# Kernel tuning notes

Hardware: AMD Instinct MI355X
Metric: run time of the kernel (lower is better)

Reference implementation:

```python
import jax, jax.numpy as jnp
import numpy as np

TOPK, NUM_CLASSES, ALPHA, BETA = 13, 80, 1.0, 6.0
IOU_EPS = 1e-7


def _cxcywh_to_xyxy(b):
    cx, cy, w, h = b[..., 0], b[..., 1], b[..., 2], b[..., 3]
    return cx - w / 2, cy - h / 2, cx + w / 2, cy + h / 2


def _pairwise_iou(pd, gt):
    # pd: [B,A,4] cxcywh, gt: [B,G,4] cxcywh -> iou [B,A,G]
    p1x, p1y, p2x, p2y = _cxcywh_to_xyxy(pd)
    g1x, g1y, g2x, g2y = _cxcywh_to_xyxy(gt)
    ix1 = jnp.maximum(p1x[:, :, None], g1x[:, None, :])
    iy1 = jnp.maximum(p1y[:, :, None], g1y[:, None, :])
    ix2 = jnp.minimum(p2x[:, :, None], g2x[:, None, :])
    iy2 = jnp.minimum(p2y[:, :, None], g2y[:, None, :])
    inter = jnp.clip(ix2 - ix1, 0) * jnp.clip(iy2 - iy1, 0)
    area_p = (p2x - p1x) * (p2y - p1y)  # [B,A]
    area_g = (g2x - g1x) * (g2y - g1y)  # [B,G]
    union = area_p[:, :, None] + area_g[:, None, :] - inter + IOU_EPS
    return inter / union


def setup_inputs() -> dict:
    key = jax.random.key(0)
    ks = jax.random.split(key, 8)
    B, A, G, C = 32, 8400, 64, 80
    img = 640.0
    pd_scores = jax.random.normal(ks[0], (B, A, C), dtype=jnp.float32)
    pd_cxy = jax.random.uniform(ks[1], (B, A, 2)) * img
    pd_wh = jax.random.uniform(ks[2], (B, A, 2)) * 115.0 + 5.0
    pd_bboxes = jnp.concatenate([pd_cxy, pd_wh], axis=-1).astype(jnp.float32)
    anc_points = (jax.random.uniform(ks[3], (A, 2)) * img).astype(jnp.float32)
    gt_labels = jax.random.randint(ks[4], (B, G, 1), 0, C, dtype=jnp.int32)
    gt_cxy = jax.random.uniform(ks[5], (B, G, 2)) * img
    gt_wh = jax.random.uniform(ks[6], (B, G, 2)) * 115.0 + 5.0
    gt_bboxes = jnp.concatenate([gt_cxy, gt_wh], axis=-1).astype(jnp.float32)
    mask_gt = jax.random.uniform(ks[7], (B, G, 1)) < 0.7  # bool
    return {"pd_scores": pd_scores, "pd_bboxes": pd_bboxes, "anc_points": anc_points,
            "gt_labels": gt_labels, "gt_bboxes": gt_bboxes, "mask_gt": mask_gt}


def reference(pd_scores, pd_bboxes, anc_points, gt_labels, gt_bboxes, mask_gt):
    B, A, C = pd_scores.shape
    G = gt_bboxes.shape[1]
    valid = mask_gt[..., 0].astype(bool)          # [B,G]
    labels = gt_labels[..., 0].astype(jnp.int32)  # [B,G]

    overlaps = _pairwise_iou(pd_bboxes, gt_bboxes)                 # [B,A,G]
    onehot_gt = jax.nn.one_hot(labels, C, dtype=pd_scores.dtype)   # [B,G,C]
    score_gt = jnp.einsum('bac,bgc->bag', pd_scores, onehot_gt)    # gather score at gt class
    metrics = jax.nn.sigmoid(score_gt) ** ALPHA * overlaps ** BETA  # [B,A,G], >= 0
    metrics = jnp.where(valid[:, None, :], metrics, -1.0)          # invalid gt -> sentinel

    # top-k anchors per gt (dim over anchors)
    _, topk_idx = jax.lax.top_k(jnp.swapaxes(metrics, 1, 2), TOPK)  # [B,G,k]
    b_ix = jnp.arange(B)[:, None, None]
    g_ix = jnp.arange(G)[None, :, None]
    cand = jnp.zeros((B, A, G), dtype=bool).at[b_ix, topk_idx, g_ix].set(True)
    cand = cand & valid[:, None, :]

    # (last such gt under ties, matching sequential overwrite order);
    # otherwise the first candidate gt keeps the anchor.
    anchor_max = metrics.max(axis=-1)                               # [B,A]
    is_max_cand = (metrics >= anchor_max[..., None]) & cand         # [B,A,G]
    has_max = is_max_cand.any(axis=-1)
    last_max = (G - 1) - jnp.argmax(is_max_cand[:, :, ::-1].astype(jnp.int32), axis=-1)
    first_cand = jnp.argmax(cand.astype(jnp.int32), axis=-1)
    assigned = jnp.where(has_max, last_max, first_cand)             # [B,A]
    fg = cand.any(axis=-1)                                          # [B,A] bool

    asg_label = jnp.take_along_axis(labels, assigned, axis=1)                   # [B,A]
    asg_bbox = jnp.take_along_axis(gt_bboxes, assigned[:, :, None], axis=1)     # [B,A,4]
    asg_iou = jnp.take_along_axis(overlaps, assigned[:, :, None], axis=2)[..., 0]  # [B,A]

    oh = jax.nn.one_hot(asg_label, C, dtype=pd_scores.dtype)
    fgf = fg.astype(pd_scores.dtype)
    target_labels = oh * fgf[..., None]
    target_bboxes = asg_bbox * fgf[..., None]
    target_scores = oh * (asg_iou * fgf)[..., None]
    return target_labels, target_bboxes, target_scores, fg
```

## Files before the change

kernel.cpp:

```cpp
#include <hip/hip_runtime.h>

#define NB 32
#define NA 8400
#define NG 64
#define NC 80
#define NK 13
#define TILE0 64
#define NT0 132

#define OFF_LBL  0
#define OFF_BBOX 21504000
#define OFF_SCR  22579200
#define OFF_FG   44083200

#define WS_METRICS_OFF 0
#define WS_METRICS_SZ  (32ull*64*8400*4)
#define WS_MASK_OFF    WS_METRICS_SZ
#define WS_MASK_SZ     (32ull*8400*8)
#define WS_NEEDED      (WS_METRICS_SZ + WS_MASK_SZ)

__device__ __forceinline__ float sigmoid_f(float x) {
    return 1.0f / (1.0f + expf(-x));
}

__device__ __forceinline__ float iou_corners(
    float px1, float py1, float px2, float py2, float ap,
    float gx1, float gy1, float gx2, float gy2, float ag)
{
    float ix1 = fmaxf(px1, gx1), iy1 = fmaxf(py1, gy1);
    float ix2 = fminf(px2, gx2), iy2 = fminf(py2, gy2);
    float inter = fmaxf(ix2 - ix1, 0.0f) * fmaxf(iy2 - iy1, 0.0f);
    return inter / (ap + ag - inter + 1e-7f);
}

__global__ __launch_bounds__(256) void metrics_kernel(
    const float* __restrict__ pd_scores,
    const float* __restrict__ pd_bboxes,
    const int* __restrict__ gt_labels,
    const float* __restrict__ gt_bboxes,
    const int* __restrict__ mask_gt,
    float* __restrict__ metrics)
{
    const int b  = blockIdx.y;
    const int a0 = blockIdx.x * TILE0;
    const int tid = threadIdx.x;
    const int an = min(TILE0, NA - a0);

    __shared__ float s_sc[TILE0 * 81];
    __shared__ float s_pb[TILE0 * 5];
    __shared__ float s_gb[NG * 5];
    __shared__ int   s_lab[NG];
    __shared__ int   s_val[NG];

    const float* sbase = pd_scores + ((size_t)b * NA + a0) * NC;
    for (int i4 = tid; i4 < an * 20; i4 += 256) {
        const float4 v = reinterpret_cast<const float4*>(sbase)[i4];
        const int al = i4 / 20;
        const int c  = (i4 % 20) * 4;
        float* d = &s_sc[al * 81 + c];
        d[0] = sigmoid_f(v.x); d[1] = sigmoid_f(v.y);
        d[2] = sigmoid_f(v.z); d[3] = sigmoid_f(v.w);
    }
    if (tid < an) {
        const float4 pb = *reinterpret_cast<const float4*>(pd_bboxes + ((size_t)b * NA + a0 + tid) * 4);
        const float px1 = pb.x - pb.z * 0.5f, py1 = pb.y - pb.w * 0.5f;
        const float px2 = pb.x + pb.z * 0.5f, py2 = pb.y + pb.w * 0.5f;
        s_pb[tid * 5 + 0] = px1; s_pb[tid * 5 + 1] = py1;
        s_pb[tid * 5 + 2] = px2; s_pb[tid * 5 + 3] = py2;
        s_pb[tid * 5 + 4] = (px2 - px1) * (py2 - py1);
    }
    if (tid >= 64 && tid < 64 + NG) {
        const int g = tid - 64;
        const float4 gb = *reinterpret_cast<const float4*>(gt_bboxes + ((size_t)b * NG + g) * 4);
        const float gx1 = gb.x - gb.z * 0.5f, gy1 = gb.y - gb.w * 0.5f;
        const float gx2 = gb.x + gb.z * 0.5f, gy2 = gb.y + gb.w * 0.5f;
        s_gb[g * 5 + 0] = gx1; s_gb[g * 5 + 1] = gy1;
        s_gb[g * 5 + 2] = gx2; s_gb[g * 5 + 3] = gy2;
        s_gb[g * 5 + 4] = (gx2 - gx1) * (gy2 - gy1);
        s_lab[g] = gt_labels[b * NG + g];
        s_val[g] = mask_gt[b * NG + g];
    }
    __syncthreads();

    const int a_local = tid & 63;
    const int ggrp    = tid >> 6;
    if (a_local < an) {
        const float px1 = s_pb[a_local * 5 + 0], py1 = s_pb[a_local * 5 + 1];
        const float px2 = s_pb[a_local * 5 + 2], py2 = s_pb[a_local * 5 + 3];
        const float ap  = s_pb[a_local * 5 + 4];
        #pragma unroll 4
        for (int gg = 0; gg < 16; ++gg) {
            const int g = gg * 4 + ggrp;
            float m = -1.0f;
            if (s_val[g]) {
                const float iou = iou_corners(px1, py1, px2, py2, ap,
                                              s_gb[g*5+0], s_gb[g*5+1], s_gb[g*5+2], s_gb[g*5+3], s_gb[g*5+4]);
                const float i2 = iou * iou;
                m = s_sc[a_local * 81 + s_lab[g]] * (i2 * i2 * i2);
            }
            metrics[((size_t)(b * NG + g)) * NA + a0 + a_local] = m;
        }
    }
}

__global__ __launch_bounds__(256) void topk_kernel(
    const float* __restrict__ metrics,
    const int* __restrict__ mask_gt,
    unsigned long long* __restrict__ cand_mask)
{
    const int g = blockIdx.x;
    const int b = blockIdx.y;
    const int tid = threadIdx.x;

    if (mask_gt[b * NG + g] == 0) return;

    __shared__ float sm[NA];
    __shared__ float wv[4];
    __shared__ int   wi[4];
    __shared__ int   s_sel[NK];

    const float* mrow = metrics + (size_t)(b * NG + g) * NA;
    for (int a = tid; a < NA; a += 256) sm[a] = mrow[a];
    __syncthreads();

    for (int k = 0; k < NK; ++k) {
        float bv = -3.0f;
        int   bi = 0x7fffffff;
        for (int a = tid; a < NA; a += 256) {
            const float v = sm[a];
            if (v > bv || (v == bv && a < bi)) { bv = v; bi = a; }
        }
        #pragma unroll
        for (int off = 32; off; off >>= 1) {
            const float ov = __shfl_xor(bv, off);
            const int   oi = __shfl_xor(bi, off);
            if (ov > bv || (ov == bv && oi < bi)) { bv = ov; bi = oi; }
        }
        const int wave = tid >> 6;
        if ((tid & 63) == 0) { wv[wave] = bv; wi[wave] = bi; }
        __syncthreads();
        if (tid == 0) {
            #pragma unroll
            for (int w = 1; w < 4; ++w) {
                if (wv[w] > bv || (wv[w] == bv && wi[w] < bi)) { bv = wv[w]; bi = wi[w]; }
            }
            s_sel[k] = bi;
            sm[bi] = -2.0f;
        }
        __syncthreads();
    }
    if (tid < NK) {
        atomicOr(&cand_mask[(size_t)b * NA + s_sel[tid]], 1ull << g);
    }
}

__global__ __launch_bounds__(256) void assign_kernel(
    const float* __restrict__ metrics,
    const float* __restrict__ pd_bboxes,
    const int* __restrict__ gt_labels,
    const float* __restrict__ gt_bboxes,
    const unsigned long long* __restrict__ cand_mask,
    float* __restrict__ out)
{
    const int b = blockIdx.y;
    const int a0 = blockIdx.x * 256;
    const int tid = threadIdx.x;
    const int a = a0 + tid;
    const bool active = a < NA;

    __shared__ float s_gb[NG * 5];
    __shared__ float s_graw[NG][4];
    __shared__ int   s_lab[NG];
    __shared__ int   s_albl[256];
    __shared__ float s_aiou[256];

    if (tid < NG) {
        const float4 gb = *reinterpret_cast<const float4*>(gt_bboxes + ((size_t)b * NG + tid) * 4);
        s_graw[tid][0] = gb.x; s_graw[tid][1] = gb.y; s_graw[tid][2] = gb.z; s_graw[tid][3] = gb.w;
        const float gx1 = gb.x - gb.z * 0.5f, gy1 = gb.y - gb.w * 0.5f;
        const float gx2 = gb.x + gb.z * 0.5f, gy2 = gb.y + gb.w * 0.5f;
        s_gb[tid * 5 + 0] = gx1; s_gb[tid * 5 + 1] = gy1;
        s_gb[tid * 5 + 2] = gx2; s_gb[tid * 5 + 3] = gy2;
        s_gb[tid * 5 + 4] = (gx2 - gx1) * (gy2 - gy1);
        s_lab[tid] = gt_labels[b * NG + tid];
    }
    __syncthreads();

    unsigned long long cand = 0ull;
    float maxv = -2.0f;
    int   last = -1;
    if (active) {
        cand = cand_mask[(size_t)b * NA + a];
        const float* mcol = metrics + (size_t)b * NG * NA + a;
        for (int g = 0; g < NG; ++g) {
            const float mv = mcol[(size_t)g * NA];
            const bool cb = (cand >> g) & 1ull;
            if (mv > maxv)       { maxv = mv; last = cb ? g : -1; }
            else if (mv == maxv && cb) { last = g; }
        }
    }

    const bool fg = (cand != 0ull);
    int assigned = 0;
    float aiou = 0.0f;
    if (fg) {
        assigned = (last >= 0) ? last : (__ffsll(cand) - 1);
        const float4 pb = *reinterpret_cast<const float4*>(pd_bboxes + ((size_t)b * NA + a) * 4);
        const float px1 = pb.x - pb.z * 0.5f, py1 = pb.y - pb.w * 0.5f;
        const float px2 = pb.x + pb.z * 0.5f, py2 = pb.y + pb.w * 0.5f;
        const float ap = (px2 - px1) * (py2 - py1);
        aiou = iou_corners(px1, py1, px2, py2, ap,
                           s_gb[assigned*5+0], s_gb[assigned*5+1],
                           s_gb[assigned*5+2], s_gb[assigned*5+3], s_gb[assigned*5+4]);
    }

    s_albl[tid] = fg ? s_lab[assigned] : -1;
    s_aiou[tid] = fg ? aiou : 0.0f;

    if (active) {
        float4 ob = fg ? make_float4(s_graw[assigned][0], s_graw[assigned][1],
                                     s_graw[assigned][2], s_graw[assigned][3])
                       : make_float4(0.f, 0.f, 0.f, 0.f);
        *reinterpret_cast<float4*>(out + OFF_BBOX + ((size_t)b * NA + a) * 4) = ob;
        out[OFF_FG + (size_t)b * NA + a] = fg ? 1.0f : 0.0f;
    }
    __syncthreads();

    const int cnt = min(256, NA - a0);
    for (int i = tid; i < cnt * NC; i += 256) {
        const int al = i / NC;
        const int c  = i - al * NC;
        const int lbl = s_albl[al];
        const float lv = (c == lbl) ? 1.0f : 0.0f;
        const float sv = (c == lbl) ? s_aiou[al] : 0.0f;
        const size_t base = ((size_t)b * NA + (a0 + al)) * NC + c;
        out[OFF_LBL + base] = lv;
        out[OFF_SCR + base] = sv;
    }
}

__global__ __launch_bounds__(256) void topk_fb(
    const float* __restrict__ pd_scores, const float* __restrict__ pd_bboxes,
    const int* __restrict__ gt_labels, const float* __restrict__ gt_bboxes,
    const int* __restrict__ mask_gt, int* __restrict__ topk_idx)
{
    const int g = blockIdx.x, b = blockIdx.y, tid = threadIdx.x;
    int* outp = topk_idx + (b * NG + g) * NK;
    if (mask_gt[b * NG + g] == 0) { if (tid < NK) outp[tid] = -1; return; }
    __shared__ float sm[NA];
    __shared__ float wv[4]; __shared__ int wi[4];
    const int label = gt_labels[b * NG + g];
    const float4 gb = *reinterpret_cast<const float4*>(gt_bboxes + (size_t)(b * NG + g) * 4);
    const float gx1 = gb.x - gb.z * 0.5f, gy1 = gb.y - gb.w * 0.5f;
    const float gx2 = gb.x + gb.z * 0.5f, gy2 = gb.y + gb.w * 0.5f;
    const float ag = (gx2 - gx1) * (gy2 - gy1);
    for (int a = tid; a < NA; a += 256) {
        const float4 pb = *reinterpret_cast<const float4*>(pd_bboxes + ((size_t)b * NA + a) * 4);
        const float px1 = pb.x - pb.z * 0.5f, py1 = pb.y - pb.w * 0.5f;
        const float px2 = pb.x + pb.z * 0.5f, py2 = pb.y + pb.w * 0.5f;
        const float ap = (px2 - px1) * (py2 - py1);
        const float iou = iou_corners(px1, py1, px2, py2, ap, gx1, gy1, gx2, gy2, ag);
        const float s = pd_scores[((size_t)b * NA + a) * NC + label];
        const float i2 = iou * iou;
        sm[a] = sigmoid_f(s) * (i2 * i2 * i2);
    }
    __syncthreads();
    for (int k = 0; k < NK; ++k) {
        float bv = -3.0f; int bi = 0x7fffffff;
        for (int a = tid; a < NA; a += 256) {
            const float v = sm[a];
            if (v > bv || (v == bv && a < bi)) { bv = v; bi = a; }
        }
        #pragma unroll
        for (int off = 32; off; off >>= 1) {
            const float ov = __shfl_xor(bv, off); const int oi = __shfl_xor(bi, off);
            if (ov > bv || (ov == bv && oi < bi)) { bv = ov; bi = oi; }
        }
        if ((tid & 63) == 0) { wv[tid >> 6] = bv; wi[tid >> 6] = bi; }
        __syncthreads();
        if (tid == 0) {
            #pragma unroll
            for (int w = 1; w < 4; ++w)
                if (wv[w] > bv || (wv[w] == bv && wi[w] < bi)) { bv = wv[w]; bi = wi[w]; }
            outp[k] = bi; sm[bi] = -2.0f;
        }
        __syncthreads();
    }
}

__global__ __launch_bounds__(256) void assign_fb(
    const float* __restrict__ pd_scores, const float* __restrict__ pd_bboxes,
    const int* __restrict__ gt_labels, const float* __restrict__ gt_bboxes,
    const int* __restrict__ mask_gt, const int* __restrict__ topk_idx,
    float* __restrict__ out)
{
    const int b = blockIdx.y, a0 = blockIdx.x * 256, tid = threadIdx.x;
    __shared__ float s_gx1[NG], s_gy1[NG], s_gx2[NG], s_gy2[NG], s_gar[NG];
    __shared__ float s_graw[NG][4];
    __shared__ int s_lab[NG], s_val[NG], s_tk[NG][NK], s_albl[256];
    __shared__ float s_aiou[256];
    if (tid < NG) {
        const float4 gb = *reinterpret_cast<const float4*>(gt_bboxes + ((size_t)b * NG + tid) * 4);
        s_graw[tid][0] = gb.x; s_graw[tid][1] = gb.y; s_graw[tid][2] = gb.z; s_graw[tid][3] = gb.w;
        const float gx1 = gb.x - gb.z * 0.5f, gy1 = gb.y - gb.w * 0.5f;
        const float gx2 = gb.x + gb.z * 0.5f, gy2 = gb.y + gb.w * 0.5f;
        s_gx1[tid] = gx1; s_gy1[tid] = gy1; s_gx2[tid] = gx2; s_gy2[tid] = gy2;
        s_gar[tid] = (gx2 - gx1) * (gy2 - gy1);
        s_lab[tid] = gt_labels[b * NG + tid];
        s_val[tid] = mask_gt[b * NG + tid];
    }
    for (int i = tid; i < NG * NK; i += 256) s_tk[i / NK][i % NK] = topk_idx[(size_t)b * NG * NK + i];
    __syncthreads();
    const int a = a0 + tid;
    const bool active = a < NA;
    float anchor_max = -1.0f;
    unsigned long long cand = 0ull;
    float px1 = 0, py1 = 0, px2 = 0, py2 = 0, ap = 0;
    const float* srow = pd_scores + ((size_t)b * NA + a) * NC;
    if (active) {
        const float4 pb = *reinterpret_cast<const float4*>(pd_bboxes + ((size_t)b * NA + a) * 4);
        px1 = pb.x - pb.z * 0.5f; py1 = pb.y - pb.w * 0.5f;
        px2 = pb.x + pb.z * 0.5f; py2 = pb.y + pb.w * 0.5f;
        ap = (px2 - px1) * (py2 - py1);
        for (int g = 0; g < NG; ++g) {
            if (!s_val[g]) continue;
            const float iou = iou_corners(px1, py1, px2, py2, ap, s_gx1[g], s_gy1[g], s_gx2[g], s_gy2[g], s_gar[g]);
            const float i2 = iou * iou;
            const float m = sigmoid_f(srow[s_lab[g]]) * (i2 * i2 * i2);
            anchor_max = fmaxf(anchor_max, m);
            bool c = false;
            #pragma unroll
            for (int k = 0; k < NK; ++k) c = c || (s_tk[g][k] == a);
            if (c) cand |= (1ull << g);
        }
    }
    const bool fg = (cand != 0ull);
    int assigned = 0; float aiou = 0.0f;
    if (fg) {
        const int first = __ffsll(cand) - 1;
        int lastg = -1;
        unsigned long long rem = cand;
        while (rem) {
            const int g = __ffsll(rem) - 1; rem &= rem - 1;
            const float iou = iou_corners(px1, py1, px2, py2, ap, s_gx1[g], s_gy1[g], s_gx2[g], s_gy2[g], s_gar[g]);
            const float i2 = iou * iou;
            const float m = sigmoid_f(srow[s_lab[g]]) * (i2 * i2 * i2);
            if (m >= anchor_max) lastg = g;
        }
        assigned = (lastg >= 0) ? lastg : first;
        aiou = iou_corners(px1, py1, px2, py2, ap, s_gx1[assigned], s_gy1[assigned], s_gx2[assigned], s_gy2[assigned], s_gar[assigned]);
    }
    s_albl[tid] = fg ? s_lab[assigned] : -1;
    s_aiou[tid] = fg ? aiou : 0.0f;
    if (active) {
        float4 ob = fg ? make_float4(s_graw[assigned][0], s_graw[assigned][1], s_graw[assigned][2], s_graw[assigned][3])
                       : make_float4(0.f, 0.f, 0.f, 0.f);
        *reinterpret_cast<float4*>(out + OFF_BBOX + ((size_t)b * NA + a) * 4) = ob;
        out[OFF_FG + (size_t)b * NA + a] = fg ? 1.0f : 0.0f;
    }
    __syncthreads();
    const int cnt = min(256, NA - a0);
    for (int i = tid; i < cnt * NC; i += 256) {
        const int al = i / NC, c = i - al * NC;
        const int lbl = s_albl[al];
        const size_t base = ((size_t)b * NA + (a0 + al)) * NC + c;
        out[OFF_LBL + base] = (c == lbl) ? 1.0f : 0.0f;
        out[OFF_SCR + base] = (c == lbl) ? s_aiou[al] : 0.0f;
    }
}

extern "C" void kernel_launch(void* const* d_in, const int* in_sizes, int n_in,
                              void* d_out, int out_size, void* d_ws, size_t ws_size,
                              hipStream_t stream) {
    const float* pd_scores = (const float*)d_in[0];
    const float* pd_bboxes = (const float*)d_in[1];
    const int*   gt_labels = (const int*)d_in[3];
    const float* gt_bboxes = (const float*)d_in[4];
    const int*   mask_gt   = (const int*)d_in[5];
    float* out = (float*)d_out;

    if (ws_size >= WS_NEEDED) {
        float* metrics = (float*)((char*)d_ws + WS_METRICS_OFF);
        unsigned long long* cmask = (unsigned long long*)((char*)d_ws + WS_MASK_OFF);

        hipMemsetAsync(cmask, 0, WS_MASK_SZ, stream);

        dim3 g0(NT0, NB);
        metrics_kernel<<<g0, 256, 0, stream>>>(pd_scores, pd_bboxes, gt_labels, gt_bboxes, mask_gt, metrics);

        dim3 g1(NG, NB);
        topk_kernel<<<g1, 256, 0, stream>>>(metrics, mask_gt, cmask);

        dim3 g2((NA + 255) / 256, NB);
        assign_kernel<<<g2, 256, 0, stream>>>(metrics, pd_bboxes, gt_labels, gt_bboxes, cmask, out);
    } else {
        int* topk = (int*)d_ws;
        dim3 g1(NG, NB);
        topk_fb<<<g1, 256, 0, stream>>>(pd_scores, pd_bboxes, gt_labels, gt_bboxes, mask_gt, topk);
        dim3 g2((NA + 255) / 256, NB);
        assign_fb<<<g2, 256, 0, stream>>>(pd_scores, pd_bboxes, gt_labels, gt_bboxes, mask_gt, topk, out);
    }
}
```

Before: 402.3 us.

## Use per-thread register top-k, precompute anchor max, vectorize one-hot stores

The top-k kernel no longer copies each metrics row to shared memory and rescans it 13 times. Each thread now keeps a sorted register list of its 13 best values, and a 13-round wave/block merge pops the winner. The metrics kernel also computes the per-anchor maximum over gts and zeroes the candidate mask, which removes the memset. The assign kernel then reads metrics only for candidate gts instead of all 64, and writes the one-hot outputs as float4. The cost is higher register pressure in top-k and an extra workspace array.

```diff
diff --git a/kernel.cpp b/kernel.cpp
--- a/kernel.cpp
+++ b/kernel.cpp
@@ -13,11 +13,10 @@
 #define OFF_SCR  22579200
 #define OFF_FG   44083200
 
-#define WS_METRICS_OFF 0
 #define WS_METRICS_SZ  (32ull*64*8400*4)
-#define WS_MASK_OFF    WS_METRICS_SZ
 #define WS_MASK_SZ     (32ull*8400*8)
-#define WS_NEEDED      (WS_METRICS_SZ + WS_MASK_SZ)
+#define WS_AMAX_SZ     (32ull*8400*4)
+#define WS_NEEDED      (WS_METRICS_SZ + WS_MASK_SZ + WS_AMAX_SZ)
 
 __device__ __forceinline__ float sigmoid_f(float x) {
     return 1.0f / (1.0f + expf(-x));
@@ -39,7 +38,9 @@
     const int* __restrict__ gt_labels,
     const float* __restrict__ gt_bboxes,
     const int* __restrict__ mask_gt,
-    float* __restrict__ metrics)
+    float* __restrict__ metrics,
+    float* __restrict__ amax_arr,
+    unsigned long long* __restrict__ cmask)
 {
     const int b  = blockIdx.y;
     const int a0 = blockIdx.x * TILE0;
@@ -49,6 +50,7 @@
     __shared__ float s_sc[TILE0 * 81];
     __shared__ float s_pb[TILE0 * 5];
     __shared__ float s_gb[NG * 5];
+    __shared__ float s_pm[4][TILE0];
     __shared__ int   s_lab[NG];
     __shared__ int   s_val[NG];
 
@@ -84,6 +86,7 @@
 
     const int a_local = tid & 63;
     const int ggrp    = tid >> 6;
+    float pm = -1.0f;
     if (a_local < an) {
         const float px1 = s_pb[a_local * 5 + 0], py1 = s_pb[a_local * 5 + 1];
         const float px2 = s_pb[a_local * 5 + 2], py2 = s_pb[a_local * 5 + 3];
@@ -98,8 +101,17 @@
                 const float i2 = iou * iou;
                 m = s_sc[a_local * 81 + s_lab[g]] * (i2 * i2 * i2);
             }
+            pm = fmaxf(pm, m);
             metrics[((size_t)(b * NG + g)) * NA + a0 + a_local] = m;
         }
+    }
+    s_pm[ggrp][a_local] = pm;
+    __syncthreads();
+    if (tid < an) {
+        const float am = fmaxf(fmaxf(s_pm[0][tid], s_pm[1][tid]),
+                               fmaxf(s_pm[2][tid], s_pm[3][tid]));
+        amax_arr[(size_t)b * NA + a0 + tid] = am;
+        cmask[(size_t)b * NA + a0 + tid] = 0ull;
     }
 }
 
@@ -114,41 +126,59 @@
 
     if (mask_gt[b * NG + g] == 0) return;
 
-    __shared__ float sm[NA];
-    __shared__ float wv[4];
-    __shared__ int   wi[4];
+    const float* __restrict__ mrow = metrics + (size_t)(b * NG + g) * NA;
+
+    float v[NK]; int ix[NK];
+    #pragma unroll
+    for (int k = 0; k < NK; ++k) { v[k] = -3.0f; ix[k] = 0x7fffffff; }
+
+    for (int base = tid * 4; base < NA; base += 1024) {
+        const float4 m4 = *reinterpret_cast<const float4*>(mrow + base);
+        const float mv4[4] = {m4.x, m4.y, m4.z, m4.w};
+        #pragma unroll
+        for (int j = 0; j < 4; ++j) {
+            float m = mv4[j];
+            int   a = base + j;
+            if (m > v[NK-1]) {
+                #pragma unroll
+                for (int k = 0; k < NK; ++k) {
+                    if (m > v[k]) {
+                        const float tv = v[k]; v[k] = m;  m = tv;
+                        const int   ti = ix[k]; ix[k] = a; a = ti;
+                    }
+                }
+            }
+        }
+    }
+
+    __shared__ float s_wv[4];
+    __shared__ int   s_wi[4];
     __shared__ int   s_sel[NK];
 
-    const float* mrow = metrics + (size_t)(b * NG + g) * NA;
-    for (int a = tid; a < NA; a += 256) sm[a] = mrow[a];
-    __syncthreads();
-
-    for (int k = 0; k < NK; ++k) {
-        float bv = -3.0f;
-        int   bi = 0x7fffffff;
-        for (int a = tid; a < NA; a += 256) {
-            const float v = sm[a];
-            if (v > bv || (v == bv && a < bi)) { bv = v; bi = a; }
-        }
+    for (int r = 0; r < NK; ++r) {
+        float bv = v[0]; int bi = ix[0];
         #pragma unroll
         for (int off = 32; off; off >>= 1) {
             const float ov = __shfl_xor(bv, off);
             const int   oi = __shfl_xor(bi, off);
             if (ov > bv || (ov == bv && oi < bi)) { bv = ov; bi = oi; }
         }
-        const int wave = tid >> 6;
-        if ((tid & 63) == 0) { wv[wave] = bv; wi[wave] = bi; }
+        if ((tid & 63) == 0) { s_wv[tid >> 6] = bv; s_wi[tid >> 6] = bi; }
         __syncthreads();
-        if (tid == 0) {
+        bv = s_wv[0]; bi = s_wi[0];
+        #pragma unroll
+        for (int w = 1; w < 4; ++w) {
+            if (s_wv[w] > bv || (s_wv[w] == bv && s_wi[w] < bi)) { bv = s_wv[w]; bi = s_wi[w]; }
+        }
+        if (tid == 0) s_sel[r] = bi;
+        if (v[0] == bv && ix[0] == bi) {
             #pragma unroll
-            for (int w = 1; w < 4; ++w) {
-                if (wv[w] > bv || (wv[w] == bv && wi[w] < bi)) { bv = wv[w]; bi = wi[w]; }
-            }
-            s_sel[k] = bi;
-            sm[bi] = -2.0f;
+            for (int k = 0; k < NK - 1; ++k) { v[k] = v[k+1]; ix[k] = ix[k+1]; }
+            v[NK-1] = -3.0f; ix[NK-1] = 0x7fffffff;
         }
         __syncthreads();
     }
+
     if (tid < NK) {
         atomicOr(&cand_mask[(size_t)b * NA + s_sel[tid]], 1ull << g);
     }
@@ -156,6 +186,7 @@
 
 __global__ __launch_bounds__(256) void assign_kernel(
     const float* __restrict__ metrics,
+    const float* __restrict__ amax_arr,
     const float* __restrict__ pd_bboxes,
     const int* __restrict__ gt_labels,
     const float* __restrict__ gt_bboxes,
@@ -187,24 +218,23 @@
     __syncthreads();
 
     unsigned long long cand = 0ull;
-    float maxv = -2.0f;
-    int   last = -1;
-    if (active) {
-        cand = cand_mask[(size_t)b * NA + a];
-        const float* mcol = metrics + (size_t)b * NG * NA + a;
-        for (int g = 0; g < NG; ++g) {
-            const float mv = mcol[(size_t)g * NA];
-            const bool cb = (cand >> g) & 1ull;
-            if (mv > maxv)       { maxv = mv; last = cb ? g : -1; }
-            else if (mv == maxv && cb) { last = g; }
-        }
-    }
-
+    if (active) cand = cand_mask[(size_t)b * NA + a];
     const bool fg = (cand != 0ull);
+
     int assigned = 0;
     float aiou = 0.0f;
     if (fg) {
-        assigned = (last >= 0) ? last : (__ffsll(cand) - 1);
+        const float am = amax_arr[(size_t)b * NA + a];
+        const int first = __ffsll(cand) - 1;
+        int last = -1;
+        unsigned long long rem = cand;
+        while (rem) {
+            const int g = __ffsll(rem) - 1;
+            rem &= rem - 1;
+            const float mv = metrics[((size_t)(b * NG + g)) * NA + a];
+            if (mv >= am) last = g;
+        }
+        assigned = (last >= 0) ? last : first;
         const float4 pb = *reinterpret_cast<const float4*>(pd_bboxes + ((size_t)b * NA + a) * 4);
         const float px1 = pb.x - pb.z * 0.5f, py1 = pb.y - pb.w * 0.5f;
         const float px2 = pb.x + pb.z * 0.5f, py2 = pb.y + pb.w * 0.5f;
@@ -227,15 +257,20 @@
     __syncthreads();
 
     const int cnt = min(256, NA - a0);
-    for (int i = tid; i < cnt * NC; i += 256) {
-        const int al = i / NC;
-        const int c  = i - al * NC;
+    float4* __restrict__ lblp = reinterpret_cast<float4*>(out + OFF_LBL + ((size_t)b * NA + a0) * NC);
+    float4* __restrict__ scrp = reinterpret_cast<float4*>(out + OFF_SCR + ((size_t)b * NA + a0) * NC);
+    for (int i4 = tid; i4 < cnt * 20; i4 += 256) {
+        const int al = i4 / 20;
+        const int cb = (i4 - al * 20) * 4;
         const int lbl = s_albl[al];
-        const float lv = (c == lbl) ? 1.0f : 0.0f;
-        const float sv = (c == lbl) ? s_aiou[al] : 0.0f;
-        const size_t base = ((size_t)b * NA + (a0 + al)) * NC + c;
-        out[OFF_LBL + base] = lv;
-        out[OFF_SCR + base] = sv;
+        const float aio = s_aiou[al];
+        float4 l4, s4;
+        l4.x = (cb + 0 == lbl) ? 1.0f : 0.0f;  s4.x = (cb + 0 == lbl) ? aio : 0.0f;
+        l4.y = (cb + 1 == lbl) ? 1.0f : 0.0f;  s4.y = (cb + 1 == lbl) ? aio : 0.0f;
+        l4.z = (cb + 2 == lbl) ? 1.0f : 0.0f;  s4.z = (cb + 2 == lbl) ? aio : 0.0f;
+        l4.w = (cb + 3 == lbl) ? 1.0f : 0.0f;  s4.w = (cb + 3 == lbl) ? aio : 0.0f;
+        lblp[i4] = l4;
+        scrp[i4] = s4;
     }
 }
 
@@ -268,8 +303,8 @@
     for (int k = 0; k < NK; ++k) {
         float bv = -3.0f; int bi = 0x7fffffff;
         for (int a = tid; a < NA; a += 256) {
-            const float v = sm[a];
-            if (v > bv || (v == bv && a < bi)) { bv = v; bi = a; }
+            const float vv = sm[a];
+            if (vv > bv || (vv == bv && a < bi)) { bv = vv; bi = a; }
         }
         #pragma unroll
         for (int off = 32; off; off >>= 1) {
@@ -380,19 +415,20 @@
     float* out = (float*)d_out;
 
     if (ws_size >= WS_NEEDED) {
-        float* metrics = (float*)((char*)d_ws + WS_METRICS_OFF);
-        unsigned long long* cmask = (unsigned long long*)((char*)d_ws + WS_MASK_OFF);
-
-        hipMemsetAsync(cmask, 0, WS_MASK_SZ, stream);
+        float* metrics = (float*)d_ws;
+        unsigned long long* cmask = (unsigned long long*)((char*)d_ws + WS_METRICS_SZ);
+        float* amax_arr = (float*)((char*)d_ws + WS_METRICS_SZ + WS_MASK_SZ);
 
         dim3 g0(NT0, NB);
-        metrics_kernel<<<g0, 256, 0, stream>>>(pd_scores, pd_bboxes, gt_labels, gt_bboxes, mask_gt, metrics);
+        metrics_kernel<<<g0, 256, 0, stream>>>(pd_scores, pd_bboxes, gt_labels, gt_bboxes,
+                                               mask_gt, metrics, amax_arr, cmask);
 
         dim3 g1(NG, NB);
         topk_kernel<<<g1, 256, 0, stream>>>(metrics, mask_gt, cmask);
 
         dim3 g2((NA + 255) / 256, NB);
-        assign_kernel<<<g2, 256, 0, stream>>>(metrics, pd_bboxes, gt_labels, gt_bboxes, cmask, out);
+        assign_kernel<<<g2, 256, 0, stream>>>(metrics, amax_arr, pd_bboxes, gt_labels, gt_bboxes,
+                                              cmask, out);
     } else {
         int* topk = (int*)d_ws;
         dim3 g1(NG, NB);
```

Measured after the change: 367.8 us. -8.6%, faster.
